# Kernel tuning notes

Measured on AMD Instinct MI355X. Metric: run time of the kernel, lower is better.

The kernel has to match this reference:

```python
import jax, jax.numpy as jnp
import numpy as np

HIDDEN = 2048
N_HEADS = 32
N_KV_HEADS = 8
HEAD_DIM = HIDDEN // N_HEADS  # 64
ROPE_BASE = 10000.0
B, S = 2, 2048
NEG_INF = -1e9


def rotate_half(x):
    x1, x2 = jnp.split(x, 2, axis=-1)
    return jnp.concatenate((-x2, x1), axis=-1)


def rope_cos_sin(seq_len, head_dim, base, dtype):
    inv_freq = 1.0 / (base ** (jnp.arange(0, head_dim, 2, dtype=jnp.float32) / head_dim))
    pos = jnp.arange(seq_len, dtype=jnp.float32)
    freqs = jnp.outer(pos, inv_freq)              # [S, D/2]
    emb = jnp.concatenate((freqs, freqs), axis=-1)  # [S, D]
    return jnp.cos(emb).astype(dtype)[None, None], jnp.sin(emb).astype(dtype)[None, None]


def setup_inputs() -> dict:
    key = jax.random.key(0)
    ks = jax.random.split(key, 5)
    hidden_states = jax.random.normal(ks[0], (B, S, HIDDEN), dtype=jnp.float32)
    # causal additive mask, Llama-style
    causal = jnp.tril(jnp.ones((S, S), dtype=bool))
    attention_mask = jnp.where(causal, 0.0, NEG_INF).astype(jnp.float32)
    attention_mask = jnp.broadcast_to(attention_mask[None, None], (B, 1, S, S))
    sc = 1.0 / np.sqrt(HIDDEN)
    Wq = jax.random.normal(ks[1], (HIDDEN, HIDDEN), dtype=jnp.float32) * sc
    Wk = jax.random.normal(ks[2], (N_KV_HEADS * HEAD_DIM, HIDDEN), dtype=jnp.float32) * sc
    Wv = jax.random.normal(ks[3], (N_KV_HEADS * HEAD_DIM, HIDDEN), dtype=jnp.float32) * sc
    Wo = jax.random.normal(ks[4], (HIDDEN, HIDDEN), dtype=jnp.float32) * sc
    return {"hidden_states": hidden_states, "attention_mask": attention_mask,
            "Wq": Wq, "Wk": Wk, "Wv": Wv, "Wo": Wo}


def reference(hidden_states, attention_mask, Wq, Wk, Wv, Wo):
    b, s, _ = hidden_states.shape
    groups = N_HEADS // N_KV_HEADS
    # projections (torch Linear: x @ W.T)
    q = (hidden_states @ Wq.T).reshape(b, s, N_HEADS, HEAD_DIM).transpose(0, 2, 1, 3)      # [b,H,s,d]
    k = (hidden_states @ Wk.T).reshape(b, s, N_KV_HEADS, HEAD_DIM).transpose(0, 2, 1, 3)   # [b,Hk,s,d]
    v = (hidden_states @ Wv.T).reshape(b, s, N_KV_HEADS, HEAD_DIM).transpose(0, 2, 1, 3)
    cos, sin = rope_cos_sin(s, HEAD_DIM, ROPE_BASE, hidden_states.dtype)
    q = q * cos + rotate_half(q) * sin
    k = k * cos + rotate_half(k) * sin
    # GQA without materializing repeated K/V: view q as [b, Hk, g, s, d]
    qg = q.reshape(b, N_KV_HEADS, groups, s, HEAD_DIM)
    scores = jnp.einsum('bhgqd,bhkd->bhgqk', qg, k) / np.sqrt(HEAD_DIM)  # [b,Hk,g,s,s]
    scores = scores + attention_mask[:, :, None]                          # mask [b,1,1,s,s]
    probs = jax.nn.softmax(scores.astype(jnp.float32), axis=-1).astype(q.dtype)
    attn = jnp.einsum('bhgqk,bhkd->bhgqd', probs, v)                      # [b,Hk,g,s,d]
    attn = attn.reshape(b, N_HEADS, s, HEAD_DIM).transpose(0, 2, 1, 3).reshape(b, s, HIDDEN)
    return attn @ Wo.T
```

## Files before the change

### kernel.cpp

```cpp
#include <hip/hip_runtime.h>
#include <math.h>

#define HID 2048
#define NH 32
#define NKV 8
#define HD 64
#define BB 2
#define SS 2048
#define MTOT (BB * SS)

typedef __bf16 bf16;
typedef __bf16 bf16x8 __attribute__((ext_vector_type(8)));
typedef __bf16 bf16x4 __attribute__((ext_vector_type(4)));
typedef float f32x4 __attribute__((ext_vector_type(4)));

#define MFMA16(a, b, c) __builtin_amdgcn_mfma_f32_16x16x32_bf16((a), (b), (c), 0, 0, 0)

__device__ __forceinline__ void load_lds16(const void* g, void* l) {
  __builtin_amdgcn_global_load_lds((const __attribute__((address_space(1))) void*)g,
                                   (__attribute__((address_space(3))) void*)l, 16, 0, 0);
}

__global__ void cvt_all(const float* __restrict__ hs, const float* __restrict__ Wq,
                        const float* __restrict__ Wk, const float* __restrict__ Wv,
                        const float* __restrict__ Wo,
                        bf16* __restrict__ A_b, bf16* __restrict__ Wq_b,
                        bf16* __restrict__ Wk_b, bf16* __restrict__ Wv_b,
                        bf16* __restrict__ Wo_b) {
  int bid = blockIdx.x;
  const float* src;
  bf16* dst;
  if (bid < 8192)       { src = hs; dst = A_b; }
  else if (bid < 12288) { src = Wq; dst = Wq_b; bid -= 8192; }
  else if (bid < 13312) { src = Wk; dst = Wk_b; bid -= 12288; }
  else if (bid < 14336) { src = Wv; dst = Wv_b; bid -= 13312; }
  else                  { src = Wo; dst = Wo_b; bid -= 14336; }
  int i = (bid * 256 + threadIdx.x) * 4;
  float4 v = *(const float4*)(src + i);
  bf16x4 o;
  o[0] = (bf16)v.x; o[1] = (bf16)v.y; o[2] = (bf16)v.z; o[3] = (bf16)v.w;
  *(bf16x4*)(dst + i) = o;
}

__device__ __forceinline__ void gemm128_core(const bf16* __restrict__ Ap,
                                             const bf16* __restrict__ Wp,
                                             bf16* As, bf16* Bs, f32x4 acc[4][4]) {
  const int tid = threadIdx.x;
  const int w = tid >> 6, lane = tid & 63;
  const int sr = lane >> 2;
  const int scc = (lane & 3) * 8;
  const int l16 = lane & 15, quad = lane >> 4;
  const int mw = (w >> 1) * 64, nw = (w & 1) * 64;

  const bf16* gA = Ap + (size_t)(w * 32 + sr) * HID + scc;
  const bf16* gB = Wp + (size_t)(w * 32 + sr) * HID + scc;
  bf16* lA = As + (w * 32) * 32;
  bf16* lB = Bs + (w * 32) * 32;

  for (int k0 = 0; k0 < HID; k0 += 32) {
    load_lds16(gA + k0, lA);
    load_lds16(gA + k0 + (size_t)16 * HID, lA + 16 * 32);
    load_lds16(gB + k0, lB);
    load_lds16(gB + k0 + (size_t)16 * HID, lB + 16 * 32);
    __syncthreads();
    bf16x8 af[4], bfr[4];
#pragma unroll
    for (int mi = 0; mi < 4; ++mi)
      af[mi] = *(const bf16x8*)&As[(mw + mi * 16 + l16) * 32 + quad * 8];
#pragma unroll
    for (int ni = 0; ni < 4; ++ni)
      bfr[ni] = *(const bf16x8*)&Bs[(nw + ni * 16 + l16) * 32 + quad * 8];
#pragma unroll
    for (int mi = 0; mi < 4; ++mi)
#pragma unroll
      for (int ni = 0; ni < 4; ++ni)
        acc[mi][ni] = MFMA16(af[mi], bfr[ni], acc[mi][ni]);
    __syncthreads();
  }
}

#define QSCALE 0.1803368801f
#define L2B 0.4152410118f
__global__ __launch_bounds__(256) void gemm_qkv(const bf16* __restrict__ A,
                                                const bf16* __restrict__ Wq,
                                                const bf16* __restrict__ Wk,
                                                const bf16* __restrict__ Wv,
                                                bf16* __restrict__ Qb,
                                                bf16* __restrict__ Kb,
                                                bf16* __restrict__ Vt) {
  __shared__ bf16 As[128 * 32];
  __shared__ bf16 Bs[128 * 32];
  const int tileM = blockIdx.x * 128;
  const int n0 = blockIdx.y * 128;
  const bf16* Wp;
  int mode;
  if (n0 < HID) { Wp = Wq + (size_t)n0 * HID; mode = 0; }
  else if (n0 < HID + 512) { Wp = Wk + (size_t)(n0 - HID) * HID; mode = 1; }
  else { Wp = Wv + (size_t)(n0 - HID - 512) * HID; mode = 2; }

  f32x4 acc[4][4];
#pragma unroll
  for (int i = 0; i < 4; ++i)
#pragma unroll
    for (int j = 0; j < 4; ++j) acc[i][j] = (f32x4){0.f, 0.f, 0.f, 0.f};

  gemm128_core(A + (size_t)tileM * HID, Wp, As, Bs, acc);

  const int tid = threadIdx.x;
  const int w = tid >> 6, lane = tid & 63;
  const int l16 = lane & 15, quad = lane >> 4;
  const int mw = (w >> 1) * 64, nw = (w & 1) * 64;

  if (mode == 2) {
#pragma unroll
    for (int mi = 0; mi < 4; ++mi)
#pragma unroll
      for (int ni = 0; ni < 4; ++ni)
#pragma unroll
        for (int r = 0; r < 4; ++r) {
          int grow = tileM + mw + mi * 16 + quad * 4 + r;
          int gcol = n0 + nw + ni * 16 + l16;
          int b = grow >> 11, spos = grow & (SS - 1);
          int nv = gcol - HID - 512;
          Vt[(((size_t)(b * NKV + (nv >> 6))) * HD + (nv & 63)) * SS + spos] =
              (bf16)acc[mi][ni][r];
        }
  } else {
    const float inv0 = __builtin_amdgcn_exp2f(-(float)l16 * L2B);
    const float inv1 = __builtin_amdgcn_exp2f(-(float)(l16 + 16) * L2B);
#pragma unroll
    for (int mi = 0; mi < 4; ++mi) {
#pragma unroll
      for (int r = 0; r < 4; ++r) {
        int grow = tileM + mw + mi * 16 + quad * 4 + r;
        int b = grow >> 11, spos = grow & (SS - 1);
        float sn0, cs0, sn1, cs1;
        sincosf((float)spos * inv0, &sn0, &cs0);
        sincosf((float)spos * inv1, &sn1, &cs1);
        float a0 = acc[mi][0][r], a1 = acc[mi][1][r];
        float a2 = acc[mi][2][r], a3 = acc[mi][3][r];
        float o0 = a0 * cs0 - a2 * sn0;
        float o2 = a2 * cs0 + a0 * sn0;
        float o1 = a1 * cs1 - a3 * sn1;
        float o3 = a3 * cs1 + a1 * sn1;
        if (mode == 0) {
          bf16* qp = Qb + (size_t)grow * HID + n0 + nw + l16;
          qp[0]  = (bf16)(o0 * QSCALE);
          qp[16] = (bf16)(o1 * QSCALE);
          qp[32] = (bf16)(o2 * QSCALE);
          qp[48] = (bf16)(o3 * QSCALE);
        } else {
          int kvh = (n0 - HID + nw) >> 6;
          bf16* kp = Kb + ((size_t)(b * NKV + kvh) * SS + spos) * HD + l16;
          kp[0]  = (bf16)o0;
          kp[16] = (bf16)o1;
          kp[32] = (bf16)o2;
          kp[48] = (bf16)o3;
        }
      }
    }
  }
}

__global__ __launch_bounds__(256) void gemm_out(const bf16* __restrict__ A,
                                                const bf16* __restrict__ Wo,
                                                float* __restrict__ out) {
  __shared__ bf16 As[128 * 32];
  __shared__ bf16 Bs[128 * 32];
  const int tileM = blockIdx.x * 128;
  const int n0 = blockIdx.y * 128;
  f32x4 acc[4][4];
#pragma unroll
  for (int i = 0; i < 4; ++i)
#pragma unroll
    for (int j = 0; j < 4; ++j) acc[i][j] = (f32x4){0.f, 0.f, 0.f, 0.f};

  gemm128_core(A + (size_t)tileM * HID, Wo + (size_t)n0 * HID, As, Bs, acc);

  const int tid = threadIdx.x;
  const int w = tid >> 6, lane = tid & 63;
  const int l16 = lane & 15, quad = lane >> 4;
  const int mw = (w >> 1) * 64, nw = (w & 1) * 64;
#pragma unroll
  for (int mi = 0; mi < 4; ++mi)
#pragma unroll
    for (int ni = 0; ni < 4; ++ni)
#pragma unroll
      for (int r = 0; r < 4; ++r) {
        int grow = tileM + mw + mi * 16 + quad * 4 + r;
        int gcol = n0 + nw + ni * 16 + l16;
        out[(size_t)grow * HID + gcol] = acc[mi][ni][r];
      }
}

#define PSTR 72
__global__ __launch_bounds__(256, 3) void attn(const bf16* __restrict__ Qb,
                                               const bf16* __restrict__ Kb,
                                               const bf16* __restrict__ Vt,
                                               bf16* __restrict__ Ctx) {
  __shared__ bf16 Ktile[2][64 * 64];
  __shared__ bf16 Vtile[2][64 * 64];
  __shared__ bf16 Pbuf[4][16 * PSTR];
  const int tid = threadIdx.x;
  const int w = tid >> 6, lane = tid & 63;
  const int l16 = lane & 15, quad = lane >> 4;
  const int bh = blockIdx.y, b = bh >> 5, h = bh & 31, kvh = h >> 2;
  bf16* Pw = &Pbuf[w][0];
  const char* Kslice = (const char*)(Kb + ((size_t)(b * NKV + kvh)) * SS * HD);
  const char* Vslice = (const char*)(Vt + ((size_t)(b * NKV + kvh)) * HD * SS);
  const int qrel = w * 16 + l16;

  const int srow = (lane >> 3) & 7;
  const int pchunk = ((lane & 7) ^ srow) << 4;
  const int so = ((quad ^ (l16 & 7)) << 4);
  const int so2 = so ^ 64;

  const int qtA = (int)blockIdx.x;

  int cur = 0;
  {
#pragma unroll
    for (int i = 0; i < 2; ++i) {
      const int r = w * 16 + i * 8 + srow;
      load_lds16(Kslice + (size_t)r * 128 + pchunk,
                 (char*)Ktile[0] + (w * 16 + i * 8) * 128);
      load_lds16(Vslice + (size_t)r * 4096 + pchunk,
                 (char*)Vtile[0] + (w * 16 + i * 8) * 128);
    }
  }

  for (int t = 0; t < 2; ++t) {
    const int qt = t ? (31 - qtA) : qtA;
    const int q = qt * 64 + qrel;

    const bf16* Qp = Qb + ((size_t)(b * SS + q)) * HID + h * HD + quad * 8;
    bf16x8 qb0 = *(const bf16x8*)Qp;
    bf16x8 qb1 = *(const bf16x8*)(Qp + 32);

    float l = 0.f;
    f32x4 oacc[4];
#pragma unroll
    for (int d = 0; d < 4; ++d) oacc[d] = (f32x4){0.f, 0.f, 0.f, 0.f};

    for (int kt = 0; kt <= qt; ++kt) {
      __syncthreads();

      const bool have_next = (kt < qt) || (t == 0);
      if (have_next) {
        const int nkb = (kt < qt) ? (kt + 1) * 64 : 0;
        const int nb = cur ^ 1;
#pragma unroll
        for (int i = 0; i < 2; ++i) {
          const int r = w * 16 + i * 8 + srow;
          load_lds16(Kslice + (size_t)(nkb + r) * 128 + pchunk,
                     (char*)Ktile[nb] + (w * 16 + i * 8) * 128);
          load_lds16(Vslice + (size_t)r * 4096 + (size_t)nkb * 2 + pchunk,
                     (char*)Vtile[nb] + (w * 16 + i * 8) * 128);
        }
      }

      const char* Kc = (const char*)Ktile[cur] + l16 * 128;
      const char* Vc = (const char*)Vtile[cur] + l16 * 128;
      const bool diag = (kt == qt);

#pragma unroll
      for (int nt = 0; nt < 4; ++nt) {
        bf16x8 kf0 = *(const bf16x8*)(Kc + nt * 2048 + so);
        bf16x8 kf1 = *(const bf16x8*)(Kc + nt * 2048 + so2);
        f32x4 s = {0.f, 0.f, 0.f, 0.f};
        s = MFMA16(kf0, qb0, s);
        s = MFMA16(kf1, qb1, s);
        bf16x4 pk;
        if (diag) {
          const int krel = nt * 16 + quad * 4;
#pragma unroll
          for (int r = 0; r < 4; ++r) {
            float p = (krel + r > qrel) ? 0.f : __builtin_amdgcn_exp2f(s[r]);
            l += p;
            pk[r] = (bf16)p;
          }
        } else {
#pragma unroll
          for (int r = 0; r < 4; ++r) {
            float p = __builtin_amdgcn_exp2f(s[r]);
            l += p;
            pk[r] = (bf16)p;
          }
        }
        *(bf16x4*)&Pw[l16 * PSTR + nt * 16 + quad * 4] = pk;
      }

      bf16x8 p0 = *(const bf16x8*)&Pw[l16 * PSTR + quad * 8];
      bf16x8 p1 = *(const bf16x8*)&Pw[l16 * PSTR + 32 + quad * 8];
#pragma unroll
      for (int dn = 0; dn < 4; ++dn) {
        bf16x8 v0 = *(const bf16x8*)(Vc + dn * 2048 + so);
        bf16x8 v1 = *(const bf16x8*)(Vc + dn * 2048 + so2);
        oacc[dn] = MFMA16(v0, p0, oacc[dn]);
        oacc[dn] = MFMA16(v1, p1, oacc[dn]);
      }
      cur ^= 1;
    }

    l += __shfl_xor(l, 16);
    l += __shfl_xor(l, 32);
    const float inv = 1.0f / l;
    bf16* Cp = Ctx + ((size_t)(b * SS + q)) * HID + h * HD + quad * 4;
#pragma unroll
    for (int dn = 0; dn < 4; ++dn) {
      bf16x4 ov;
#pragma unroll
      for (int r = 0; r < 4; ++r) ov[r] = (bf16)(oacc[dn][r] * inv);
      *(bf16x4*)(Cp + dn * 16) = ov;
    }
  }
}

extern "C" void kernel_launch(void* const* d_in, const int* in_sizes, int n_in,
                              void* d_out, int out_size, void* d_ws, size_t ws_size,
                              hipStream_t stream) {
  const float* hs = (const float*)d_in[0];
  const float* Wq = (const float*)d_in[2];
  const float* Wk = (const float*)d_in[3];
  const float* Wv = (const float*)d_in[4];
  const float* Wo = (const float*)d_in[5];

  char* ws = (char*)d_ws;
  bf16* A_b  = (bf16*)(ws);
  bf16* Wq_b = (bf16*)(ws + 16777216);
  bf16* Wk_b = (bf16*)(ws + 25165824);
  bf16* Wv_b = (bf16*)(ws + 27262976);
  bf16* Wo_b = (bf16*)(ws + 29360128);
  bf16* Qb   = (bf16*)(ws + 37748736);
  bf16* Kb   = (bf16*)(ws + 54525952);
  bf16* Vt   = (bf16*)(ws + 58720256);
  bf16* Ctx  = A_b;

  cvt_all<<<18432, 256, 0, stream>>>(hs, Wq, Wk, Wv, Wo, A_b, Wq_b, Wk_b, Wv_b, Wo_b);
  gemm_qkv<<<dim3(MTOT / 128, 24), 256, 0, stream>>>(A_b, Wq_b, Wk_b, Wv_b, Qb, Kb, Vt);
  attn<<<dim3(16, BB * NH), 256, 0, stream>>>(Qb, Kb, Vt, Ctx);
  gemm_out<<<dim3(MTOT / 128, HID / 128), 256, 0, stream>>>(Ctx, Wo_b, (float*)d_out);
}
```

Before: 337.3 us.

## Rewrite GEMM core with triple-buffered LDS pipeline, swizzle, and larger tiles

```diff
diff --git a/kernel.cpp b/kernel.cpp
--- a/kernel.cpp
+++ b/kernel.cpp
@@ -20,6 +20,12 @@
   __builtin_amdgcn_global_load_lds((const __attribute__((address_space(1))) void*)g,
                                    (__attribute__((address_space(3))) void*)l, 16, 0, 0);
 }
+
+#define FENCE() asm volatile("" ::: "memory")
+#define BARX() do { FENCE(); __builtin_amdgcn_s_barrier(); FENCE(); } while (0)
+#define SYNC_VM(N) do { FENCE(); \
+  asm volatile("s_waitcnt vmcnt(" #N ") lgkmcnt(0)" ::: "memory"); \
+  __builtin_amdgcn_s_barrier(); FENCE(); } while (0)
 
 __global__ void cvt_all(const float* __restrict__ hs, const float* __restrict__ Wq,
                         const float* __restrict__ Wk, const float* __restrict__ Wv,
@@ -42,86 +48,129 @@
   *(bf16x4*)(dst + i) = o;
 }
 
-__device__ __forceinline__ void gemm128_core(const bf16* __restrict__ Ap,
-                                             const bf16* __restrict__ Wp,
-                                             bf16* As, bf16* Bs, f32x4 acc[4][4]) {
+template <int MR>
+__device__ __forceinline__ void gemm_core(const char* Agc, const char* Bgc,
+                                          char* lds, f32x4 (&acc)[MR][4]) {
+  constexpr int ABYTES = MR * 32 * 64;
+  constexpr int BUFB = ABYTES + 16384;
+  constexpr int NT = HID / 32;
+
   const int tid = threadIdx.x;
   const int w = tid >> 6, lane = tid & 63;
-  const int sr = lane >> 2;
-  const int scc = (lane & 3) * 8;
   const int l16 = lane & 15, quad = lane >> 4;
-  const int mw = (w >> 1) * 64, nw = (w & 1) * 64;
-
-  const bf16* gA = Ap + (size_t)(w * 32 + sr) * HID + scc;
-  const bf16* gB = Wp + (size_t)(w * 32 + sr) * HID + scc;
-  bf16* lA = As + (w * 32) * 32;
-  bf16* lB = Bs + (w * 32) * 32;
-
-  for (int k0 = 0; k0 < HID; k0 += 32) {
-    load_lds16(gA + k0, lA);
-    load_lds16(gA + k0 + (size_t)16 * HID, lA + 16 * 32);
-    load_lds16(gB + k0, lB);
-    load_lds16(gB + k0 + (size_t)16 * HID, lB + 16 * 32);
-    __syncthreads();
-    bf16x8 af[4], bfr[4];
-#pragma unroll
-    for (int mi = 0; mi < 4; ++mi)
-      af[mi] = *(const bf16x8*)&As[(mw + mi * 16 + l16) * 32 + quad * 8];
+  const int wr = w >> 2, wc = w & 3;
+  const int wb = w * 1024;
+
+  const int cu = (tid & 7) ^ ((tid >> 3) & 7);
+  const int srcR0 = 2 * (tid >> 3) + (cu >> 2);
+  const int srcC = (cu & 3) * 16;
+  const char* gA = Agc + (size_t)srcR0 * (HID * 2) + srcC;
+  const char* gB = Bgc + (size_t)srcR0 * (HID * 2) + srcC;
+
+  const int acg16 = ((((l16 & 1) << 2) | quad) ^ ((l16 >> 1) & 7)) * 16;
+  const int aoff = (wr * (MR * 8) + (l16 >> 1)) * 128 + acg16;
+  const int boff = (wc * 32 + (l16 >> 1)) * 128 + acg16;
+
+#pragma unroll
+  for (int t0 = 0; t0 < 2; ++t0) {
+    char* lb = lds + t0 * BUFB;
+    load_lds16(gA + t0 * 64, lb + wb);
+    if constexpr (MR == 8)
+      load_lds16(gA + (size_t)128 * (HID * 2) + t0 * 64, lb + 8192 + wb);
+    load_lds16(gB + t0 * 64, lb + ABYTES + wb);
+    load_lds16(gB + (size_t)128 * (HID * 2) + t0 * 64, lb + ABYTES + 8192 + wb);
+  }
+
+  char* cur = lds;
+  char* stg = lds + 2 * BUFB;
+  for (int kt = 0; kt < NT; ++kt) {
+    if constexpr (MR == 8) SYNC_VM(4); else SYNC_VM(3);
+    const int ks = (kt + 2 <= NT - 1) ? (kt + 2) * 64 : (NT - 1) * 64;
+    const char* Ac = cur;
+    const char* Bc = cur + ABYTES;
+
+    load_lds16(gA + ks, stg + wb);
+    load_lds16(gB + ks, stg + ABYTES + wb);
+    bf16x8 bfr[4];
 #pragma unroll
     for (int ni = 0; ni < 4; ++ni)
-      bfr[ni] = *(const bf16x8*)&Bs[(nw + ni * 16 + l16) * 32 + quad * 8];
-#pragma unroll
-    for (int mi = 0; mi < 4; ++mi)
+      bfr[ni] = *(const bf16x8*)(Bc + boff + ni * 1024);
+    bf16x8 af[MR / 2];
+#pragma unroll
+    for (int mi = 0; mi < MR / 2; ++mi)
+      af[mi] = *(const bf16x8*)(Ac + aoff + mi * 1024);
+    __builtin_amdgcn_s_setprio(1);
+#pragma unroll
+    for (int mi = 0; mi < MR / 2; ++mi)
 #pragma unroll
       for (int ni = 0; ni < 4; ++ni)
         acc[mi][ni] = MFMA16(af[mi], bfr[ni], acc[mi][ni]);
-    __syncthreads();
-  }
+    __builtin_amdgcn_s_setprio(0);
+    BARX();
+
+    if constexpr (MR == 8)
+      load_lds16(gA + (size_t)128 * (HID * 2) + ks, stg + 8192 + wb);
+    load_lds16(gB + (size_t)128 * (HID * 2) + ks, stg + ABYTES + 8192 + wb);
+#pragma unroll
+    for (int mi = 0; mi < MR / 2; ++mi)
+      af[mi] = *(const bf16x8*)(Ac + aoff + (MR / 2 + mi) * 1024);
+    __builtin_amdgcn_s_setprio(1);
+#pragma unroll
+    for (int mi = 0; mi < MR / 2; ++mi)
+#pragma unroll
+      for (int ni = 0; ni < 4; ++ni)
+        acc[MR / 2 + mi][ni] = MFMA16(af[mi], bfr[ni], acc[MR / 2 + mi][ni]);
+    __builtin_amdgcn_s_setprio(0);
+
+    cur = (cur == lds + 2 * BUFB) ? lds : cur + BUFB;
+    stg = (stg == lds + 2 * BUFB) ? lds : stg + BUFB;
+  }
+  asm volatile("s_waitcnt vmcnt(0)" ::: "memory");
 }
 
 #define QSCALE 0.1803368801f
 #define L2B 0.4152410118f
-__global__ __launch_bounds__(256) void gemm_qkv(const bf16* __restrict__ A,
-                                                const bf16* __restrict__ Wq,
-                                                const bf16* __restrict__ Wk,
-                                                const bf16* __restrict__ Wv,
-                                                bf16* __restrict__ Qb,
-                                                bf16* __restrict__ Kb,
-                                                bf16* __restrict__ Vt) {
-  __shared__ bf16 As[128 * 32];
-  __shared__ bf16 Bs[128 * 32];
-  const int tileM = blockIdx.x * 128;
-  const int n0 = blockIdx.y * 128;
+__global__ __launch_bounds__(512, 2) void gemm_qkv(const bf16* __restrict__ A,
+                                                   const bf16* __restrict__ Wq,
+                                                   const bf16* __restrict__ Wk,
+                                                   const bf16* __restrict__ Wv,
+                                                   bf16* __restrict__ Qb,
+                                                   bf16* __restrict__ Kb,
+                                                   bf16* __restrict__ Vt) {
+  __shared__ __align__(16) char lds[3 * (256 * 64 + 16384)];
+  const int tileM = blockIdx.x * 256;
+  const int n0 = blockIdx.y * 256;
   const bf16* Wp;
   int mode;
   if (n0 < HID) { Wp = Wq + (size_t)n0 * HID; mode = 0; }
   else if (n0 < HID + 512) { Wp = Wk + (size_t)(n0 - HID) * HID; mode = 1; }
   else { Wp = Wv + (size_t)(n0 - HID - 512) * HID; mode = 2; }
 
-  f32x4 acc[4][4];
-#pragma unroll
-  for (int i = 0; i < 4; ++i)
+  f32x4 acc[8][4];
+#pragma unroll
+  for (int i = 0; i < 8; ++i)
 #pragma unroll
     for (int j = 0; j < 4; ++j) acc[i][j] = (f32x4){0.f, 0.f, 0.f, 0.f};
 
-  gemm128_core(A + (size_t)tileM * HID, Wp, As, Bs, acc);
+  gemm_core<8>((const char*)(A + (size_t)tileM * HID), (const char*)Wp, lds, acc);
 
   const int tid = threadIdx.x;
   const int w = tid >> 6, lane = tid & 63;
   const int l16 = lane & 15, quad = lane >> 4;
-  const int mw = (w >> 1) * 64, nw = (w & 1) * 64;
+  const int wr = w >> 2, wc = w & 3;
+  const int mbase = tileM + wr * 128;
+  const int cb = n0 + wc * 64;
 
   if (mode == 2) {
 #pragma unroll
-    for (int mi = 0; mi < 4; ++mi)
+    for (int mi = 0; mi < 8; ++mi)
 #pragma unroll
       for (int ni = 0; ni < 4; ++ni)
 #pragma unroll
         for (int r = 0; r < 4; ++r) {
-          int grow = tileM + mw + mi * 16 + quad * 4 + r;
-          int gcol = n0 + nw + ni * 16 + l16;
+          int grow = mbase + mi * 16 + quad * 4 + r;
           int b = grow >> 11, spos = grow & (SS - 1);
-          int nv = gcol - HID - 512;
+          int nv = cb + ni * 16 + l16 - (HID + 512);
           Vt[(((size_t)(b * NKV + (nv >> 6))) * HD + (nv & 63)) * SS + spos] =
               (bf16)acc[mi][ni][r];
         }
@@ -129,10 +178,10 @@
     const float inv0 = __builtin_amdgcn_exp2f(-(float)l16 * L2B);
     const float inv1 = __builtin_amdgcn_exp2f(-(float)(l16 + 16) * L2B);
 #pragma unroll
-    for (int mi = 0; mi < 4; ++mi) {
+    for (int mi = 0; mi < 8; ++mi) {
 #pragma unroll
       for (int r = 0; r < 4; ++r) {
-        int grow = tileM + mw + mi * 16 + quad * 4 + r;
+        int grow = mbase + mi * 16 + quad * 4 + r;
         int b = grow >> 11, spos = grow & (SS - 1);
         float sn0, cs0, sn1, cs1;
         sincosf((float)spos * inv0, &sn0, &cs0);
@@ -144,13 +193,13 @@
         float o1 = a1 * cs1 - a3 * sn1;
         float o3 = a3 * cs1 + a1 * sn1;
         if (mode == 0) {
-          bf16* qp = Qb + (size_t)grow * HID + n0 + nw + l16;
+          bf16* qp = Qb + (size_t)grow * HID + cb + l16;
           qp[0]  = (bf16)(o0 * QSCALE);
           qp[16] = (bf16)(o1 * QSCALE);
           qp[32] = (bf16)(o2 * QSCALE);
           qp[48] = (bf16)(o3 * QSCALE);
         } else {
-          int kvh = (n0 - HID + nw) >> 6;
+          int kvh = (cb - HID) >> 6;
           bf16* kp = Kb + ((size_t)(b * NKV + kvh) * SS + spos) * HD + l16;
           kp[0]  = (bf16)o0;
           kp[16] = (bf16)o1;
@@ -162,33 +211,33 @@
   }
 }
 
-__global__ __launch_bounds__(256) void gemm_out(const bf16* __restrict__ A,
-                                                const bf16* __restrict__ Wo,
-                                                float* __restrict__ out) {
-  __shared__ bf16 As[128 * 32];
-  __shared__ bf16 Bs[128 * 32];
+__global__ __launch_bounds__(512, 2) void gemm_out(const bf16* __restrict__ A,
+                                                   const bf16* __restrict__ Wo,
+                                                   float* __restrict__ out) {
+  __shared__ __align__(16) char lds[3 * (128 * 64 + 16384)];
   const int tileM = blockIdx.x * 128;
-  const int n0 = blockIdx.y * 128;
+  const int n0 = blockIdx.y * 256;
   f32x4 acc[4][4];
 #pragma unroll
   for (int i = 0; i < 4; ++i)
 #pragma unroll
     for (int j = 0; j < 4; ++j) acc[i][j] = (f32x4){0.f, 0.f, 0.f, 0.f};
 
-  gemm128_core(A + (size_t)tileM * HID, Wo + (size_t)n0 * HID, As, Bs, acc);
+  gemm_core<4>((const char*)(A + (size_t)tileM * HID),
+               (const char*)(Wo + (size_t)n0 * HID), lds, acc);
 
   const int tid = threadIdx.x;
   const int w = tid >> 6, lane = tid & 63;
   const int l16 = lane & 15, quad = lane >> 4;
-  const int mw = (w >> 1) * 64, nw = (w & 1) * 64;
+  const int wr = w >> 2, wc = w & 3;
 #pragma unroll
   for (int mi = 0; mi < 4; ++mi)
 #pragma unroll
     for (int ni = 0; ni < 4; ++ni)
 #pragma unroll
       for (int r = 0; r < 4; ++r) {
-        int grow = tileM + mw + mi * 16 + quad * 4 + r;
-        int gcol = n0 + nw + ni * 16 + l16;
+        int grow = tileM + wr * 64 + mi * 16 + quad * 4 + r;
+        int gcol = n0 + wc * 64 + ni * 16 + l16;
         out[(size_t)grow * HID + gcol] = acc[mi][ni][r];
       }
 }
@@ -337,7 +386,7 @@
   bf16* Ctx  = A_b;
 
   cvt_all<<<18432, 256, 0, stream>>>(hs, Wq, Wk, Wv, Wo, A_b, Wq_b, Wk_b, Wv_b, Wo_b);
-  gemm_qkv<<<dim3(MTOT / 128, 24), 256, 0, stream>>>(A_b, Wq_b, Wk_b, Wv_b, Qb, Kb, Vt);
+  gemm_qkv<<<dim3(MTOT / 256, 12), 512, 0, stream>>>(A_b, Wq_b, Wk_b, Wv_b, Qb, Kb, Vt);
   attn<<<dim3(16, BB * NH), 256, 0, stream>>>(Qb, Kb, Vt, Ctx);
-  gemm_out<<<dim3(MTOT / 128, HID / 128), 256, 0, stream>>>(Ctx, Wo_b, (float*)d_out);
-}
+  gemm_out<<<dim3(MTOT / 128, HID / 256), 512, 0, stream>>>(Ctx, Wo_b, (float*)d_out);
+}
```

Result: faster. 319.3 us (-5.3%).

## Triple-buffer GEMM mainloop with async LDS loads and swizzled layout

Applied to the files above, without the earlier changes.

```diff
diff --git a/kernel.cpp b/kernel.cpp
--- a/kernel.cpp
+++ b/kernel.cpp
@@ -20,6 +20,11 @@
   __builtin_amdgcn_global_load_lds((const __attribute__((address_space(1))) void*)g,
                                    (__attribute__((address_space(3))) void*)l, 16, 0, 0);
 }
+
+#define FENCE() asm volatile("" ::: "memory")
+#define SYNC_VM(N) do { FENCE(); \
+  asm volatile("s_waitcnt vmcnt(" #N ") lgkmcnt(0)" ::: "memory"); \
+  __builtin_amdgcn_s_barrier(); FENCE(); } while (0)
 
 __global__ void cvt_all(const float* __restrict__ hs, const float* __restrict__ Wq,
                         const float* __restrict__ Wk, const float* __restrict__ Wv,
@@ -42,54 +47,80 @@
   *(bf16x4*)(dst + i) = o;
 }
 
-__device__ __forceinline__ void gemm128_core(const bf16* __restrict__ Ap,
-                                             const bf16* __restrict__ Wp,
-                                             bf16* As, bf16* Bs, f32x4 acc[4][4]) {
+__device__ __forceinline__ void gemm_core(const char* Agc, const char* Bgc,
+                                          char* lds, f32x4 (&acc)[4][4]) {
+  constexpr int ABYTES = 8192;
+  constexpr int BUFB = 16384;
+  constexpr int NT = HID / 32;
+
   const int tid = threadIdx.x;
   const int w = tid >> 6, lane = tid & 63;
-  const int sr = lane >> 2;
-  const int scc = (lane & 3) * 8;
   const int l16 = lane & 15, quad = lane >> 4;
-  const int mw = (w >> 1) * 64, nw = (w & 1) * 64;
-
-  const bf16* gA = Ap + (size_t)(w * 32 + sr) * HID + scc;
-  const bf16* gB = Wp + (size_t)(w * 32 + sr) * HID + scc;
-  bf16* lA = As + (w * 32) * 32;
-  bf16* lB = Bs + (w * 32) * 32;
-
-  for (int k0 = 0; k0 < HID; k0 += 32) {
-    load_lds16(gA + k0, lA);
-    load_lds16(gA + k0 + (size_t)16 * HID, lA + 16 * 32);
-    load_lds16(gB + k0, lB);
-    load_lds16(gB + k0 + (size_t)16 * HID, lB + 16 * 32);
-    __syncthreads();
+  const int wr = w >> 1, wc = w & 1;
+  const int wb = w * 1024;
+
+  const int cu = (tid & 7) ^ ((tid >> 3) & 7);
+  const int srcR0 = 2 * (tid >> 3) + (cu >> 2);
+  const int srcC = (cu & 3) * 16;
+  const char* gA = Agc + (size_t)srcR0 * (HID * 2) + srcC;
+  const char* gB = Bgc + (size_t)srcR0 * (HID * 2) + srcC;
+
+  const int acg16 = ((((l16 & 1) << 2) | quad) ^ ((l16 >> 1) & 7)) * 16;
+  const int aoff = (wr * 32 + (l16 >> 1)) * 128 + acg16;
+  const int boff = (wc * 32 + (l16 >> 1)) * 128 + acg16;
+
+#pragma unroll
+  for (int t0 = 0; t0 < 2; ++t0) {
+    char* lb = lds + t0 * BUFB;
+    load_lds16(gA + t0 * 64, lb + wb);
+    load_lds16(gA + (size_t)64 * (HID * 2) + t0 * 64, lb + 4096 + wb);
+    load_lds16(gB + t0 * 64, lb + ABYTES + wb);
+    load_lds16(gB + (size_t)64 * (HID * 2) + t0 * 64, lb + ABYTES + 4096 + wb);
+  }
+
+  char* cur = lds;
+  char* stg = lds + 2 * BUFB;
+  for (int kt = 0; kt < NT; ++kt) {
+    SYNC_VM(4);
+    const int ks = (kt + 2 < NT) ? (kt + 2) * 64 : (NT - 1) * 64;
+
+    load_lds16(gA + ks, stg + wb);
+    load_lds16(gA + (size_t)64 * (HID * 2) + ks, stg + 4096 + wb);
+    load_lds16(gB + ks, stg + ABYTES + wb);
+    load_lds16(gB + (size_t)64 * (HID * 2) + ks, stg + ABYTES + 4096 + wb);
+    FENCE();
+
     bf16x8 af[4], bfr[4];
 #pragma unroll
+    for (int ni = 0; ni < 4; ++ni)
+      bfr[ni] = *(const bf16x8*)(cur + ABYTES + boff + ni * 1024);
+#pragma unroll
     for (int mi = 0; mi < 4; ++mi)
-      af[mi] = *(const bf16x8*)&As[(mw + mi * 16 + l16) * 32 + quad * 8];
-#pragma unroll
-    for (int ni = 0; ni < 4; ++ni)
-      bfr[ni] = *(const bf16x8*)&Bs[(nw + ni * 16 + l16) * 32 + quad * 8];
+      af[mi] = *(const bf16x8*)(cur + aoff + mi * 1024);
+    __builtin_amdgcn_s_setprio(1);
 #pragma unroll
     for (int mi = 0; mi < 4; ++mi)
 #pragma unroll
       for (int ni = 0; ni < 4; ++ni)
         acc[mi][ni] = MFMA16(af[mi], bfr[ni], acc[mi][ni]);
-    __syncthreads();
-  }
+    __builtin_amdgcn_s_setprio(0);
+
+    cur = (cur == lds + 2 * BUFB) ? lds : cur + BUFB;
+    stg = (stg == lds + 2 * BUFB) ? lds : stg + BUFB;
+  }
+  asm volatile("s_waitcnt vmcnt(0)" ::: "memory");
 }
 
 #define QSCALE 0.1803368801f
 #define L2B 0.4152410118f
-__global__ __launch_bounds__(256) void gemm_qkv(const bf16* __restrict__ A,
-                                                const bf16* __restrict__ Wq,
-                                                const bf16* __restrict__ Wk,
-                                                const bf16* __restrict__ Wv,
-                                                bf16* __restrict__ Qb,
-                                                bf16* __restrict__ Kb,
-                                                bf16* __restrict__ Vt) {
-  __shared__ bf16 As[128 * 32];
-  __shared__ bf16 Bs[128 * 32];
+__global__ __launch_bounds__(256, 3) void gemm_qkv(const bf16* __restrict__ A,
+                                                   const bf16* __restrict__ Wq,
+                                                   const bf16* __restrict__ Wk,
+                                                   const bf16* __restrict__ Wv,
+                                                   bf16* __restrict__ Qb,
+                                                   bf16* __restrict__ Kb,
+                                                   bf16* __restrict__ Vt) {
+  __shared__ __align__(16) char lds[3 * 16384];
   const int tileM = blockIdx.x * 128;
   const int n0 = blockIdx.y * 128;
   const bf16* Wp;
@@ -104,12 +135,14 @@
 #pragma unroll
     for (int j = 0; j < 4; ++j) acc[i][j] = (f32x4){0.f, 0.f, 0.f, 0.f};
 
-  gemm128_core(A + (size_t)tileM * HID, Wp, As, Bs, acc);
+  gemm_core((const char*)(A + (size_t)tileM * HID), (const char*)Wp, lds, acc);
 
   const int tid = threadIdx.x;
   const int w = tid >> 6, lane = tid & 63;
   const int l16 = lane & 15, quad = lane >> 4;
   const int mw = (w >> 1) * 64, nw = (w & 1) * 64;
+  const int mbase = tileM + mw;
+  const int cb = n0 + nw;
 
   if (mode == 2) {
 #pragma unroll
@@ -118,10 +151,9 @@
       for (int ni = 0; ni < 4; ++ni)
 #pragma unroll
         for (int r = 0; r < 4; ++r) {
-          int grow = tileM + mw + mi * 16 + quad * 4 + r;
-          int gcol = n0 + nw + ni * 16 + l16;
+          int grow = mbase + mi * 16 + quad * 4 + r;
           int b = grow >> 11, spos = grow & (SS - 1);
-          int nv = gcol - HID - 512;
+          int nv = cb + ni * 16 + l16 - (HID + 512);
           Vt[(((size_t)(b * NKV + (nv >> 6))) * HD + (nv & 63)) * SS + spos] =
               (bf16)acc[mi][ni][r];
         }
@@ -132,7 +164,7 @@
     for (int mi = 0; mi < 4; ++mi) {
 #pragma unroll
       for (int r = 0; r < 4; ++r) {
-        int grow = tileM + mw + mi * 16 + quad * 4 + r;
+        int grow = mbase + mi * 16 + quad * 4 + r;
         int b = grow >> 11, spos = grow & (SS - 1);
         float sn0, cs0, sn1, cs1;
         sincosf((float)spos * inv0, &sn0, &cs0);
@@ -144,13 +176,13 @@
         float o1 = a1 * cs1 - a3 * sn1;
         float o3 = a3 * cs1 + a1 * sn1;
         if (mode == 0) {
-          bf16* qp = Qb + (size_t)grow * HID + n0 + nw + l16;
+          bf16* qp = Qb + (size_t)grow * HID + cb + l16;
           qp[0]  = (bf16)(o0 * QSCALE);
           qp[16] = (bf16)(o1 * QSCALE);
           qp[32] = (bf16)(o2 * QSCALE);
           qp[48] = (bf16)(o3 * QSCALE);
         } else {
-          int kvh = (n0 - HID + nw) >> 6;
+          int kvh = (cb - HID) >> 6;
           bf16* kp = Kb + ((size_t)(b * NKV + kvh) * SS + spos) * HD + l16;
           kp[0]  = (bf16)o0;
           kp[16] = (bf16)o1;
@@ -162,11 +194,10 @@
   }
 }
 
-__global__ __launch_bounds__(256) void gemm_out(const bf16* __restrict__ A,
-                                                const bf16* __restrict__ Wo,
-                                                float* __restrict__ out) {
-  __shared__ bf16 As[128 * 32];
-  __shared__ bf16 Bs[128 * 32];
+__global__ __launch_bounds__(256, 3) void gemm_out(const bf16* __restrict__ A,
+                                                   const bf16* __restrict__ Wo,
+                                                   float* __restrict__ out) {
+  __shared__ __align__(16) char lds[3 * 16384];
   const int tileM = blockIdx.x * 128;
   const int n0 = blockIdx.y * 128;
   f32x4 acc[4][4];
@@ -175,7 +206,8 @@
 #pragma unroll
     for (int j = 0; j < 4; ++j) acc[i][j] = (f32x4){0.f, 0.f, 0.f, 0.f};
 
-  gemm128_core(A + (size_t)tileM * HID, Wo + (size_t)n0 * HID, As, Bs, acc);
+  gemm_core((const char*)(A + (size_t)tileM * HID),
+            (const char*)(Wo + (size_t)n0 * HID), lds, acc);
 
   const int tid = threadIdx.x;
   const int w = tid >> 6, lane = tid & 63;
```

Measured after the change: 305.9 us. 9.3% less time.
